# Kernel tuning notes

Measured on AMD Instinct MI355X. Metric: run time of the kernel, lower is better.

The kernel has to match this reference:

```python
import jax, jax.numpy as jnp
import numpy as np


def _conv(x, w, b):
    # stride-2, pad-1 3x3 conv, NCHW/OIHW
    y = jax.lax.conv_general_dilated(x, w, (2, 2), [(1, 1), (1, 1)],
                                     dimension_numbers=('NCHW', 'OIHW', 'NCHW'))
    return y + b[None, :, None, None]


def _bn(x, g, b, eps=1e-5):
    # BatchNorm2d in training mode: batch statistics over (N, H, W)
    m = x.mean((0, 2, 3), keepdims=True)
    v = x.var((0, 2, 3), keepdims=True)
    return (x - m) * jax.lax.rsqrt(v + eps) * g[None, :, None, None] + b[None, :, None, None]


def setup_inputs() -> dict:
    key = jax.random.key(0)
    ks = iter(jax.random.split(key, 64))
    def rn(shape, scale):
        return jax.random.normal(next(ks), shape, jnp.float32) * scale
    d = {}
    d['img'] = jax.random.normal(next(ks), (64, 3, 128, 128), jnp.float32)
    d['qst'] = jax.random.normal(next(ks), (64, 11), jnp.float32)
    cin = 3
    for i in range(1, 5):
        d[f'cw{i}'] = rn((24, cin, 3, 3), 1.0 / np.sqrt(cin * 9))
        d[f'cb{i}'] = jnp.zeros((24,), jnp.float32)
        d[f'bg{i}'] = jnp.ones((24,), jnp.float32)
        d[f'bb{i}'] = jnp.zeros((24,), jnp.float32)
        cin = 24
    gdims = [63, 256, 256, 256]
    for i in range(1, 5):
        d[f'gw{i}'] = rn((gdims[i - 1], 256), 1.0 / np.sqrt(gdims[i - 1]))
        d[f'gb{i}'] = jnp.zeros((256,), jnp.float32)
    fdims = [(256, 256), (256, 256), (256, 10)]
    for i, (a, b) in enumerate(fdims, 1):
        d[f'fw{i}'] = rn((a, b), 1.0 / np.sqrt(a))
        d[f'fb{i}'] = jnp.zeros((b,), jnp.float32)
    return d


def reference(img, qst,
              cw1, cb1, bg1, bb1, cw2, cb2, bg2, bb2,
              cw3, cb3, bg3, bb3, cw4, cb4, bg4, bb4,
              gw1, gb1, gw2, gb2, gw3, gb3, gw4, gb4,
              fw1, fb1, fw2, fb2, fw3, fb3):
    x = img
    for cw, cb, bg, bb in ((cw1, cb1, bg1, bb1), (cw2, cb2, bg2, bb2),
                           (cw3, cb3, bg3, bb3), (cw4, cb4, bg4, bb4)):
        x = _bn(jax.nn.relu(_conv(x, cw, cb)), bg, bb)
    B, C, H, W = x.shape
    n = H * W  # number of objects (feature-map cells)
    o = x.reshape(B, C, n).transpose(0, 2, 1)  # [B, n, 24]
    idx = jnp.arange(n)
    coords = jnp.stack([idx // H, idx % W], axis=1).astype(x.dtype)  # [n, 2]
    o = jnp.concatenate([o, jnp.broadcast_to(coords, (B, n, 2))], axis=2)  # [B, n, 26]
    # First G layer fused over the pairwise concat cat([x_i, x_j, qst], -1) @ gw1:
    # x_i[b,a,c] = o[b,c], x_j[b,a,c] = o[b,a] -> split gw1 into the three blocks.
    Wi, Wj, Wq = gw1[:26], gw1[26:52], gw1[52:]
    h = jax.nn.relu((o @ Wi)[:, None, :, :]
                    + (o @ Wj)[:, :, None, :]
                    + (qst @ Wq + gb1)[:, None, None, :])  # [B, n, n, 256]
    h = jax.nn.relu(h @ gw2 + gb2)
    h = jax.nn.relu(h @ gw3 + gb3)
    h = jax.nn.relu(h @ gw4 + gb4)
    g = h.sum((1, 2))  # sum over all n*n pairs -> [B, 256]
    f = jax.nn.relu(g @ fw1 + fb1)
    f = jax.nn.relu(f @ fw2 + fb2)  # Dropout(0.5) is identity at inference
    return jax.nn.softmax(f @ fw3 + fb3, axis=-1)
```

## Files before the change

kernel.cpp:

```cpp
#include <hip/hip_runtime.h>
#include <hip/hip_bf16.h>

typedef __attribute__((ext_vector_type(8))) short bf16x8_t;
typedef __attribute__((ext_vector_type(4))) float f32x4_t;

__device__ __forceinline__ unsigned bfr(float x) {
  unsigned u = __builtin_bit_cast(unsigned, x);
  return (u + 0x7fffu + ((u >> 16) & 1u)) >> 16;
}
__device__ __forceinline__ unsigned pk2(float lo, float hi) {
  return bfr(lo) | (bfr(hi) << 16);
}

template<int CIN, int H, int COG, bool BNIN>
__global__ __launch_bounds__(256) void convk(
    const float* __restrict__ x, const float* __restrict__ wgt,
    const float* __restrict__ bias,
    const float* __restrict__ instats,
    const float* __restrict__ ing, const float* __restrict__ inb,
    float* __restrict__ y, float* __restrict__ stats)
{
  constexpr int W = H, HO = H / 2, WO = W / 2;
  constexpr int PXB = (COG == 1) ? 256 : 64;
  constexpr int OHS = PXB / WO;
  constexpr int SPB = HO / OHS;
  constexpr int NR = 2 * OHS + 1;
  constexpr int TW = W + 1;
  constexpr int NSTG = NR * W;
  constexpr int NCO = 24 / COG;

  __shared__ float tile[2][NR][TW];
  __shared__ float scb[CIN], shb[CIN];
  __shared__ float sred[24], sqd[24];

  const int tid = threadIdx.x;
  const int b = blockIdx.x / SPB;
  const int strip = blockIdx.x % SPB;
  const int oh0 = strip * OHS;
  const int lane = tid & 63;

  if (BNIN && tid < CIN) {
    const float cnt = 64.f * H * W;
    const float m = instats[tid] / cnt;
    const float v = instats[24 + tid] / cnt - m * m;
    const float s = rsqrtf(v + 1e-5f) * ing[tid];
    scb[tid] = s;
    shb[tid] = inb[tid] - m * s;
  }
  if (tid < 24) { sred[tid] = 0.f; sqd[tid] = 0.f; }
  for (int i = tid; i < 2 * NR; i += 256)
    tile[i / NR][i % NR][0] = 0.f;
  __syncthreads();

  const int px = (COG == 1) ? tid : lane;
  const int ow = px % WO;
  const int ohl = px / WO;
  const int oh = oh0 + ohl;
  const int cb = (COG == 1) ? 0
               : __builtin_amdgcn_readfirstlane(tid >> 6) * NCO;

  float acc[NCO];
  #pragma unroll
  for (int n = 0; n < NCO; ++n) acc[n] = bias[cb + n];

  {
    const float sc = BNIN ? scb[0] : 1.f, sh = BNIN ? shb[0] : 0.f;
    #pragma unroll
    for (int idx = tid; idx < NSTG; idx += 256) {
      const int c = idx % W, rl = idx / W;
      const int ih = oh0 * 2 - 1 + rl;
      float v = 0.f;
      if (ih >= 0)
        v = x[((size_t)(b * CIN + 0) * H + ih) * W + c] * sc + sh;
      tile[0][rl][c + 1] = v;
    }
  }
  __syncthreads();

  for (int ci = 0; ci < CIN; ++ci) {
    if (ci + 1 < CIN) {
      const float sc = BNIN ? scb[ci + 1] : 1.f, sh = BNIN ? shb[ci + 1] : 0.f;
      #pragma unroll
      for (int idx = tid; idx < NSTG; idx += 256) {
        const int c = idx % W, rl = idx / W;
        const int ih = oh0 * 2 - 1 + rl;
        float v = 0.f;
        if (ih >= 0)
          v = x[((size_t)(b * CIN + ci + 1) * H + ih) * W + c] * sc + sh;
        tile[(ci + 1) & 1][rl][c + 1] = v;
      }
    }
    float tp[9];
    #pragma unroll
    for (int r = 0; r < 3; ++r)
      #pragma unroll
      for (int s = 0; s < 3; ++s)
        tp[r * 3 + s] = tile[ci & 1][2 * ohl + r][2 * ow + s];
    #pragma unroll
    for (int n = 0; n < NCO; ++n) {
      const float* wp = wgt + (size_t)((cb + n) * CIN + ci) * 9;
      float a = acc[n];
      #pragma unroll
      for (int k = 0; k < 9; ++k) a += tp[k] * wp[k];
      acc[n] = a;
    }
    __syncthreads();
  }

  #pragma unroll
  for (int n = 0; n < NCO; ++n) {
    const float v = fmaxf(acc[n], 0.f);
    acc[n] = v;
    y[((size_t)(b * 24 + cb + n) * HO + oh) * WO + ow] = v;
  }
  #pragma unroll
  for (int n = 0; n < NCO; ++n) {
    float v = acc[n], q = v * v;
    #pragma unroll
    for (int d = 1; d < 64; d <<= 1) {
      v += __shfl_xor(v, d, 64);
      q += __shfl_xor(q, d, 64);
    }
    if (lane == 0) {
      atomicAdd(&sred[cb + n], v);
      atomicAdd(&sqd[cb + n], q);
    }
  }
  __syncthreads();
  if (tid < 24) {
    atomicAdd(&stats[tid], sred[tid]);
    atomicAdd(&stats[24 + tid], sqd[tid]);
  }
}

__global__ __launch_bounds__(256) void build_ab(
    const float* __restrict__ x4, const float* __restrict__ stats4,
    const float* __restrict__ g4, const float* __restrict__ b4,
    const float* __restrict__ gw1, const float* __restrict__ gb1,
    const float* __restrict__ qst,
    float* __restrict__ A, float* __restrict__ Bm, float* __restrict__ Cq)
{
  const int bp = blockIdx.x;
  const int b = bp >> 6, p = bp & 63;
  const int t = threadIdx.x;
  __shared__ float o[26];
  if (t < 24) {
    const float m = stats4[t] * (1.f / 4096.f);
    const float v = stats4[24 + t] * (1.f / 4096.f) - m * m;
    const float sc = rsqrtf(v + 1e-5f) * g4[t];
    const float sh = b4[t] - m * sc;
    o[t] = x4[(size_t)(b * 24 + t) * 64 + p] * sc + sh;
  } else if (t == 24) o[24] = (float)(p >> 3);
  else if (t == 25) o[25] = (float)(p & 7);
  __syncthreads();
  float a = 0.f, bb2 = 0.f;
  #pragma unroll
  for (int c = 0; c < 26; ++c) {
    a   += o[c] * gw1[c * 256 + t];
    bb2 += o[c] * gw1[(26 + c) * 256 + t];
  }
  A[(size_t)bp * 256 + t]  = a;
  Bm[(size_t)bp * 256 + t] = bb2;
  if (p == 0) {
    float cqa = gb1[t];
    #pragma unroll
    for (int c = 0; c < 11; ++c)
      cqa += qst[b * 11 + c] * gw1[(52 + c) * 256 + t];
    Cq[b * 256 + t] = cqa;
  }
}

__global__ __launch_bounds__(256) void wt_convert3(
    const float* __restrict__ W2, const float* __restrict__ W3,
    const float* __restrict__ W4, unsigned short* __restrict__ wt)
{
  const int which = blockIdx.x >> 6;
  const float* W = which == 0 ? W2 : which == 1 ? W3 : W4;
  unsigned short* o = wt + (size_t)which * 65536;
  __shared__ float ts[32][33];
  const int blk = blockIdx.x & 63;
  const int k0 = (blk & 7) * 32, n0 = (blk >> 3) * 32;
  const int t = threadIdx.x;
  const int r = t >> 3, c4 = (t & 7) * 4;
  const float4 v = *(const float4*)(W + (size_t)(k0 + r) * 256 + n0 + c4);
  ts[r][c4 + 0] = v.x; ts[r][c4 + 1] = v.y;
  ts[r][c4 + 2] = v.z; ts[r][c4 + 3] = v.w;
  __syncthreads();
  uint2 ov;
  ov.x = pk2(ts[c4 + 0][r], ts[c4 + 1][r]);
  ov.y = pk2(ts[c4 + 2][r], ts[c4 + 3][r]);
  *(uint2*)(o + (size_t)(n0 + r) * 256 + k0 + c4) = ov;
}

__global__ __launch_bounds__(256) void pair_mfma(
    const float* __restrict__ A, const float* __restrict__ Bm,
    const float* __restrict__ Cq,
    const unsigned short* __restrict__ wtall,
    const float* __restrict__ b2, const float* __restrict__ b3,
    const float* __restrict__ b4,
    float* __restrict__ Gpart)
{
  __shared__ __align__(16) unsigned short hsm[64 * 256];
  __shared__ __align__(16) unsigned short wbuf[2][256 * 40];
  __shared__ float gpart[256];

  const int tid = threadIdx.x;
  int bid = blockIdx.x;
  bid = (bid & 7) * 512 + (bid >> 3);
  const int b = bid >> 6, local = bid & 63;
  const int lane = tid & 63, cg = tid >> 6;
  const int l15 = lane & 15, l4 = lane >> 4;
  char* hbase = (char*)hsm;

  const int r0 = tid >> 2, ss = tid & 3;

  {
    const int m = tid >> 2, seg = tid & 3;
    const float* Ar = A  + (size_t)(b * 64 + m) * 256 + seg * 64;
    const float* Br = Bm + (size_t)(b * 64 + local) * 256 + seg * 64;
    const float* Cr = Cq + (size_t)b * 256 + seg * 64;
    #pragma unroll
    for (int it = 0; it < 8; ++it) {
      const float4 a0 = *(const float4*)(Ar + it * 8);
      const float4 a1 = *(const float4*)(Ar + it * 8 + 4);
      const float4 b0 = *(const float4*)(Br + it * 8);
      const float4 b1 = *(const float4*)(Br + it * 8 + 4);
      const float4 c0 = *(const float4*)(Cr + it * 8);
      const float4 c1 = *(const float4*)(Cr + it * 8 + 4);
      uint4 pk;
      pk.x = pk2(fmaxf(a0.x + b0.x + c0.x, 0.f), fmaxf(a0.y + b0.y + c0.y, 0.f));
      pk.y = pk2(fmaxf(a0.z + b0.z + c0.z, 0.f), fmaxf(a0.w + b0.w + c0.w, 0.f));
      pk.z = pk2(fmaxf(a1.x + b1.x + c1.x, 0.f), fmaxf(a1.y + b1.y + c1.y, 0.f));
      pk.w = pk2(fmaxf(a1.z + b1.z + c1.z, 0.f), fmaxf(a1.w + b1.w + c1.w, 0.f));
      const int kb = seg * 128 + it * 16;
      *(uint4*)(hbase + (size_t)m * 512 + (kb ^ ((m & 7) << 4))) = pk;
    }
  }

  {
    #pragma unroll
    for (int q = 0; q < 4; ++q) {
      const int n = r0 + q * 64;
      const uint4 v = *(const uint4*)(wtall + (size_t)n * 256 + ss * 8);
      *(uint4*)(wbuf[0] + n * 40 + ss * 8) = v;
    }
  }
  __syncthreads();

  const float* bs3[3] = {b2, b3, b4};

  for (int layer = 0; layer < 3; ++layer) {
    f32x4_t acc[4][4];
    #pragma unroll
    for (int a = 0; a < 4; ++a) {
      const float4 bv = *(const float4*)(bs3[layer] + cg * 64 + a * 16 + l4 * 4);
      #pragma unroll
      for (int t = 0; t < 4; ++t) {
        acc[a][t][0] = bv.x; acc[a][t][1] = bv.y;
        acc[a][t][2] = bv.z; acc[a][t][3] = bv.w;
      }
    }
    for (int ks = 0; ks < 8; ++ks) {
      const int c = layer * 8 + ks;
      uint4 p0, p1, p2, p3;
      if (c + 1 < 24) {
        const unsigned short* src =
            wtall + (size_t)((c + 1) >> 3) * 65536 + ((c + 1) & 7) * 32;
        p0 = *(const uint4*)(src + (size_t)(r0)       * 256 + ss * 8);
        p1 = *(const uint4*)(src + (size_t)(r0 + 64)  * 256 + ss * 8);
        p2 = *(const uint4*)(src + (size_t)(r0 + 128) * 256 + ss * 8);
        p3 = *(const uint4*)(src + (size_t)(r0 + 192) * 256 + ss * 8);
      }
      bf16x8_t bf[4];
      #pragma unroll
      for (int t = 0; t < 4; ++t) {
        const int row = t * 16 + l15;
        const int kb = ks * 64 + l4 * 16;
        bf[t] = *(const bf16x8_t*)(hbase + (size_t)row * 512 + (kb ^ ((row & 7) << 4)));
      }
      const unsigned short* wrd = wbuf[c & 1];
      #pragma unroll
      for (int a = 0; a < 4; ++a) {
        const bf16x8_t af = *(const bf16x8_t*)(wrd + (cg * 64 + a * 16 + l15) * 40 + l4 * 8);
        #pragma unroll
        for (int t = 0; t < 4; ++t)
          acc[a][t] = __builtin_amdgcn_mfma_f32_16x16x32_bf16(af, bf[t], acc[a][t], 0, 0, 0);
      }
      if (c + 1 < 24) {
        unsigned short* wb = wbuf[(c + 1) & 1];
        *(uint4*)(wb + (r0)       * 40 + ss * 8) = p0;
        *(uint4*)(wb + (r0 + 64)  * 40 + ss * 8) = p1;
        *(uint4*)(wb + (r0 + 128) * 40 + ss * 8) = p2;
        *(uint4*)(wb + (r0 + 192) * 40 + ss * 8) = p3;
      }
      __syncthreads();
    }

    if (layer < 2) {
      #pragma unroll
      for (int a = 0; a < 4; ++a) {
        #pragma unroll
        for (int t = 0; t < 4; ++t) {
          const int row = t * 16 + l15;
          const int n0 = cg * 64 + a * 16 + l4 * 4;
          uint2 v;
          v.x = pk2(fmaxf(acc[a][t][0], 0.f), fmaxf(acc[a][t][1], 0.f));
          v.y = pk2(fmaxf(acc[a][t][2], 0.f), fmaxf(acc[a][t][3], 0.f));
          *(uint2*)(hbase + (size_t)row * 512 + ((n0 * 2) ^ ((row & 7) << 4))) = v;
        }
      }
      __syncthreads();
    } else {
      #pragma unroll
      for (int a = 0; a < 4; ++a) {
        f32x4_t s;
        s[0] = s[1] = s[2] = s[3] = 0.f;
        #pragma unroll
        for (int t = 0; t < 4; ++t) {
          s[0] += fmaxf(acc[a][t][0], 0.f);
          s[1] += fmaxf(acc[a][t][1], 0.f);
          s[2] += fmaxf(acc[a][t][2], 0.f);
          s[3] += fmaxf(acc[a][t][3], 0.f);
        }
        #pragma unroll
        for (int d = 1; d < 16; d <<= 1) {
          s[0] += __shfl_xor(s[0], d, 64);
          s[1] += __shfl_xor(s[1], d, 64);
          s[2] += __shfl_xor(s[2], d, 64);
          s[3] += __shfl_xor(s[3], d, 64);
        }
        if (l15 == 0)
          *(f32x4_t*)(&gpart[cg * 64 + a * 16 + l4 * 4]) = s;
      }
      __syncthreads();
      Gpart[(size_t)(b * 64 + local) * 256 + tid] = gpart[tid];
    }
  }
}

__global__ __launch_bounds__(256) void reduce_g(
    const float* __restrict__ Gpart, float* __restrict__ g)
{
  const int b = blockIdx.x, t = threadIdx.x;
  float s = 0.f;
  for (int j = 0; j < 64; ++j) s += Gpart[(size_t)(b * 64 + j) * 256 + t];
  g[b * 256 + t] = s;
}

__global__ __launch_bounds__(256) void fnet(
    const float* __restrict__ g,
    const float* __restrict__ fw1, const float* __restrict__ fb1,
    const float* __restrict__ fw2, const float* __restrict__ fb2,
    const float* __restrict__ fw3, const float* __restrict__ fb3,
    float* __restrict__ out)
{
  const int b = blockIdx.x, t = threadIdx.x;
  __shared__ float s0[256], s1[256], lg[10];
  s0[t] = g[b * 256 + t];
  __syncthreads();
  float acc = fb1[t];
  for (int k = 0; k < 256; ++k) acc += s0[k] * fw1[k * 256 + t];
  s1[t] = fmaxf(acc, 0.f);
  __syncthreads();
  acc = fb2[t];
  for (int k = 0; k < 256; ++k) acc += s1[k] * fw2[k * 256 + t];
  s0[t] = fmaxf(acc, 0.f);
  __syncthreads();
  if (t < 10) {
    float a = fb3[t];
    for (int k = 0; k < 256; ++k) a += s0[k] * fw3[k * 10 + t];
    lg[t] = a;
  }
  __syncthreads();
  if (t == 0) {
    float m = lg[0];
    for (int c = 1; c < 10; ++c) m = fmaxf(m, lg[c]);
    float e[10], sum = 0.f;
    for (int c = 0; c < 10; ++c) { e[c] = expf(lg[c] - m); sum += e[c]; }
    const float inv = 1.f / sum;
    for (int c = 0; c < 10; ++c) out[b * 10 + c] = e[c] * inv;
  }
}

extern "C" void kernel_launch(void* const* d_in, const int* in_sizes, int n_in,
                              void* d_out, int out_size, void* d_ws, size_t ws_size,
                              hipStream_t stream)
{
  const float* img = (const float*)d_in[0];
  const float* qst = (const float*)d_in[1];
  const float* cw[4] = {(const float*)d_in[2],  (const float*)d_in[6],
                        (const float*)d_in[10], (const float*)d_in[14]};
  const float* cb[4] = {(const float*)d_in[3],  (const float*)d_in[7],
                        (const float*)d_in[11], (const float*)d_in[15]};
  const float* bg[4] = {(const float*)d_in[4],  (const float*)d_in[8],
                        (const float*)d_in[12], (const float*)d_in[16]};
  const float* bb[4] = {(const float*)d_in[5],  (const float*)d_in[9],
                        (const float*)d_in[13], (const float*)d_in[17]};
  const float* gw1 = (const float*)d_in[18];
  const float* gb1 = (const float*)d_in[19];
  const float* gw2 = (const float*)d_in[20];
  const float* gb2 = (const float*)d_in[21];
  const float* gw3 = (const float*)d_in[22];
  const float* gb3 = (const float*)d_in[23];
  const float* gw4 = (const float*)d_in[24];
  const float* gb4 = (const float*)d_in[25];
  const float* fw1 = (const float*)d_in[26];
  const float* fb1 = (const float*)d_in[27];
  const float* fw2 = (const float*)d_in[28];
  const float* fb2 = (const float*)d_in[29];
  const float* fw3 = (const float*)d_in[30];
  const float* fb3 = (const float*)d_in[31];
  float* out = (float*)d_out;

  float* ws    = (float*)d_ws;
  float* x1    = ws;
  float* x2    = x1 + 6291456;
  float* x3    = x2 + 1572864;
  float* x4    = x3 + 393216;
  float* Abuf  = x4 + 98304;
  float* Bbuf  = Abuf + 1048576;
  float* Cqb   = Bbuf + 1048576;
  float* Gpart = Cqb + 16384;
  float* gbuf  = Gpart + 1048576;
  float* stats = gbuf + 16384;
  unsigned short* wtb = (unsigned short*)(stats + 192);

  hipMemsetAsync(stats, 0, 192 * sizeof(float), stream);

  convk<3, 128, 1, false><<<1024, 256, 0, stream>>>(
      img, cw[0], cb[0], nullptr, nullptr, nullptr, x1, stats + 0);
  convk<24, 64, 4, true><<<1024, 256, 0, stream>>>(
      x1, cw[1], cb[1], stats + 0, bg[0], bb[0], x2, stats + 48);
  convk<24, 32, 4, true><<<256, 256, 0, stream>>>(
      x2, cw[2], cb[2], stats + 48, bg[1], bb[1], x3, stats + 96);
  convk<24, 16, 4, true><<<64, 256, 0, stream>>>(
      x3, cw[3], cb[3], stats + 96, bg[2], bb[2], x4, stats + 144);

  build_ab<<<4096, 256, 0, stream>>>(x4, stats + 144, bg[3], bb[3], gw1,
                                     gb1, qst, Abuf, Bbuf, Cqb);
  wt_convert3<<<192, 256, 0, stream>>>(gw2, gw3, gw4, wtb);

  pair_mfma<<<4096, 256, 0, stream>>>(Abuf, Bbuf, Cqb, wtb, gb2, gb3, gb4,
                                      Gpart);
  reduce_g<<<64, 256, 0, stream>>>(Gpart, gbuf);
  fnet<<<64, 256, 0, stream>>>(gbuf, fw1, fb1, fw2, fb2, fw3, fb3, out);
}
```

Baseline: 572.4 us.

## Pre-swizzle MFMA weight fragments, batch build_ab rows, fuse reduce_g into fnet

Weights for layers 2-4 are now converted into a per-k-slice MFMA fragment layout, so pair_mfma streams each slice with contiguous uint4 copies and reads A-fragments directly by lane, with no padded strided rows. build_ab handles 8 objects per block, so each gw1 weight load is reused across eight rows and the launch shrinks from 4096 blocks to 512. The separate reduce_g kernel is folded into fnet, which drops one launch and one intermediate buffer. The weight conversion now runs first in the stream, and the new LDS fragment layout may have different bank-conflict behaviour.

```diff
diff --git a/kernel.cpp b/kernel.cpp
--- a/kernel.cpp
+++ b/kernel.cpp
@@ -141,27 +141,40 @@
     float* __restrict__ A, float* __restrict__ Bm, float* __restrict__ Cq)
 {
   const int bp = blockIdx.x;
-  const int b = bp >> 6, p = bp & 63;
+  const int b = bp >> 3, pg = bp & 7;
   const int t = threadIdx.x;
-  __shared__ float o[26];
-  if (t < 24) {
-    const float m = stats4[t] * (1.f / 4096.f);
-    const float v = stats4[24 + t] * (1.f / 4096.f) - m * m;
-    const float sc = rsqrtf(v + 1e-5f) * g4[t];
-    const float sh = b4[t] - m * sc;
-    o[t] = x4[(size_t)(b * 24 + t) * 64 + p] * sc + sh;
-  } else if (t == 24) o[24] = (float)(p >> 3);
-  else if (t == 25) o[25] = (float)(p & 7);
-  __syncthreads();
-  float a = 0.f, bb2 = 0.f;
+  __shared__ float o[8][26];
+  if (t < 208) {
+    const int r = t / 26, c = t % 26;
+    if (c < 24) {
+      const float m = stats4[c] * (1.f / 4096.f);
+      const float v = stats4[24 + c] * (1.f / 4096.f) - m * m;
+      const float sc = rsqrtf(v + 1e-5f) * g4[c];
+      const float sh = b4[c] - m * sc;
+      o[r][c] = x4[(size_t)(b * 24 + c) * 64 + pg * 8 + r] * sc + sh;
+    } else if (c == 24) o[r][24] = (float)pg;
+    else                o[r][25] = (float)r;
+  }
+  __syncthreads();
+  float accA[8], accB[8];
+  #pragma unroll
+  for (int r = 0; r < 8; ++r) { accA[r] = 0.f; accB[r] = 0.f; }
   #pragma unroll
   for (int c = 0; c < 26; ++c) {
-    a   += o[c] * gw1[c * 256 + t];
-    bb2 += o[c] * gw1[(26 + c) * 256 + t];
-  }
-  A[(size_t)bp * 256 + t]  = a;
-  Bm[(size_t)bp * 256 + t] = bb2;
-  if (p == 0) {
+    const float wi = gw1[c * 256 + t];
+    const float wj = gw1[(26 + c) * 256 + t];
+    #pragma unroll
+    for (int r = 0; r < 8; ++r) {
+      accA[r] += o[r][c] * wi;
+      accB[r] += o[r][c] * wj;
+    }
+  }
+  #pragma unroll
+  for (int r = 0; r < 8; ++r) {
+    A[(size_t)(b * 64 + pg * 8 + r) * 256 + t]  = accA[r];
+    Bm[(size_t)(b * 64 + pg * 8 + r) * 256 + t] = accB[r];
+  }
+  if (pg == 0) {
     float cqa = gb1[t];
     #pragma unroll
     for (int c = 0; c < 11; ++c)
@@ -170,26 +183,28 @@
   }
 }
 
-__global__ __launch_bounds__(256) void wt_convert3(
+__global__ __launch_bounds__(256) void wt_convert_frag(
     const float* __restrict__ W2, const float* __restrict__ W3,
     const float* __restrict__ W4, unsigned short* __restrict__ wt)
 {
-  const int which = blockIdx.x >> 6;
-  const float* W = which == 0 ? W2 : which == 1 ? W3 : W4;
-  unsigned short* o = wt + (size_t)which * 65536;
-  __shared__ float ts[32][33];
-  const int blk = blockIdx.x & 63;
-  const int k0 = (blk & 7) * 32, n0 = (blk >> 3) * 32;
+  const int c = blockIdx.x;
+  const int layer = c >> 3, ks = c & 7;
+  const float* W = layer == 0 ? W2 : layer == 1 ? W3 : W4;
   const int t = threadIdx.x;
-  const int r = t >> 3, c4 = (t & 7) * 4;
-  const float4 v = *(const float4*)(W + (size_t)(k0 + r) * 256 + n0 + c4);
-  ts[r][c4 + 0] = v.x; ts[r][c4 + 1] = v.y;
-  ts[r][c4 + 2] = v.z; ts[r][c4 + 3] = v.w;
-  __syncthreads();
-  uint2 ov;
-  ov.x = pk2(ts[c4 + 0][r], ts[c4 + 1][r]);
-  ov.y = pk2(ts[c4 + 2][r], ts[c4 + 3][r]);
-  *(uint2*)(o + (size_t)(n0 + r) * 256 + k0 + c4) = ov;
+  #pragma unroll
+  for (int q = 0; q < 4; ++q) {
+    const int f = q * 256 + t;
+    const int cg = f >> 8, a = (f >> 6) & 3, ln = f & 63;
+    const int n = cg * 64 + a * 16 + (ln & 15);
+    const int k0 = ks * 32 + (ln >> 4) * 8;
+    float w[8];
+    #pragma unroll
+    for (int u = 0; u < 8; ++u) w[u] = W[(size_t)(k0 + u) * 256 + n];
+    uint4 ov;
+    ov.x = pk2(w[0], w[1]); ov.y = pk2(w[2], w[3]);
+    ov.z = pk2(w[4], w[5]); ov.w = pk2(w[6], w[7]);
+    *(uint4*)(wt + (size_t)c * 8192 + (size_t)f * 8) = ov;
+  }
 }
 
 __global__ __launch_bounds__(256) void pair_mfma(
@@ -201,7 +216,7 @@
     float* __restrict__ Gpart)
 {
   __shared__ __align__(16) unsigned short hsm[64 * 256];
-  __shared__ __align__(16) unsigned short wbuf[2][256 * 40];
+  __shared__ __align__(16) unsigned short wbuf[2][8192];
   __shared__ float gpart[256];
 
   const int tid = threadIdx.x;
@@ -211,8 +226,6 @@
   const int lane = tid & 63, cg = tid >> 6;
   const int l15 = lane & 15, l4 = lane >> 4;
   char* hbase = (char*)hsm;
-
-  const int r0 = tid >> 2, ss = tid & 3;
 
   {
     const int m = tid >> 2, seg = tid & 3;
@@ -238,12 +251,11 @@
   }
 
   {
-    #pragma unroll
-    for (int q = 0; q < 4; ++q) {
-      const int n = r0 + q * 64;
-      const uint4 v = *(const uint4*)(wtall + (size_t)n * 256 + ss * 8);
-      *(uint4*)(wbuf[0] + n * 40 + ss * 8) = v;
-    }
+    const uint4* src = (const uint4*)wtall;
+    uint4* dst = (uint4*)wbuf[0];
+    #pragma unroll
+    for (int q = 0; q < 4; ++q)
+      dst[q * 256 + tid] = src[q * 256 + tid];
   }
   __syncthreads();
 
@@ -264,12 +276,11 @@
       const int c = layer * 8 + ks;
       uint4 p0, p1, p2, p3;
       if (c + 1 < 24) {
-        const unsigned short* src =
-            wtall + (size_t)((c + 1) >> 3) * 65536 + ((c + 1) & 7) * 32;
-        p0 = *(const uint4*)(src + (size_t)(r0)       * 256 + ss * 8);
-        p1 = *(const uint4*)(src + (size_t)(r0 + 64)  * 256 + ss * 8);
-        p2 = *(const uint4*)(src + (size_t)(r0 + 128) * 256 + ss * 8);
-        p3 = *(const uint4*)(src + (size_t)(r0 + 192) * 256 + ss * 8);
+        const uint4* src = (const uint4*)wtall + (size_t)(c + 1) * 1024;
+        p0 = src[0 * 256 + tid];
+        p1 = src[1 * 256 + tid];
+        p2 = src[2 * 256 + tid];
+        p3 = src[3 * 256 + tid];
       }
       bf16x8_t bf[4];
       #pragma unroll
@@ -281,17 +292,17 @@
       const unsigned short* wrd = wbuf[c & 1];
       #pragma unroll
       for (int a = 0; a < 4; ++a) {
-        const bf16x8_t af = *(const bf16x8_t*)(wrd + (cg * 64 + a * 16 + l15) * 40 + l4 * 8);
+        const bf16x8_t af = *(const bf16x8_t*)(wrd + ((size_t)(cg * 4 + a) * 64 + lane) * 8);
         #pragma unroll
         for (int t = 0; t < 4; ++t)
           acc[a][t] = __builtin_amdgcn_mfma_f32_16x16x32_bf16(af, bf[t], acc[a][t], 0, 0, 0);
       }
       if (c + 1 < 24) {
-        unsigned short* wb = wbuf[(c + 1) & 1];
-        *(uint4*)(wb + (r0)       * 40 + ss * 8) = p0;
-        *(uint4*)(wb + (r0 + 64)  * 40 + ss * 8) = p1;
-        *(uint4*)(wb + (r0 + 128) * 40 + ss * 8) = p2;
-        *(uint4*)(wb + (r0 + 192) * 40 + ss * 8) = p3;
+        uint4* wb = (uint4*)wbuf[(c + 1) & 1];
+        wb[0 * 256 + tid] = p0;
+        wb[1 * 256 + tid] = p1;
+        wb[2 * 256 + tid] = p2;
+        wb[3 * 256 + tid] = p3;
       }
       __syncthreads();
     }
@@ -338,17 +349,8 @@
   }
 }
 
-__global__ __launch_bounds__(256) void reduce_g(
-    const float* __restrict__ Gpart, float* __restrict__ g)
-{
-  const int b = blockIdx.x, t = threadIdx.x;
-  float s = 0.f;
-  for (int j = 0; j < 64; ++j) s += Gpart[(size_t)(b * 64 + j) * 256 + t];
-  g[b * 256 + t] = s;
-}
-
 __global__ __launch_bounds__(256) void fnet(
-    const float* __restrict__ g,
+    const float* __restrict__ Gpart,
     const float* __restrict__ fw1, const float* __restrict__ fb1,
     const float* __restrict__ fw2, const float* __restrict__ fb2,
     const float* __restrict__ fw3, const float* __restrict__ fb3,
@@ -356,7 +358,10 @@
 {
   const int b = blockIdx.x, t = threadIdx.x;
   __shared__ float s0[256], s1[256], lg[10];
-  s0[t] = g[b * 256 + t];
+  float g = 0.f;
+  for (int j = 0; j < 64; ++j)
+    g += Gpart[(size_t)(b * 64 + j) * 256 + t];
+  s0[t] = g;
   __syncthreads();
   float acc = fb1[t];
   for (int k = 0; k < 256; ++k) acc += s0[k] * fw1[k * 256 + t];
@@ -421,11 +426,12 @@
   float* Bbuf  = Abuf + 1048576;
   float* Cqb   = Bbuf + 1048576;
   float* Gpart = Cqb + 16384;
-  float* gbuf  = Gpart + 1048576;
-  float* stats = gbuf + 16384;
+  float* stats = Gpart + 1048576;
   unsigned short* wtb = (unsigned short*)(stats + 192);
 
   hipMemsetAsync(stats, 0, 192 * sizeof(float), stream);
+
+  wt_convert_frag<<<24, 256, 0, stream>>>(gw2, gw3, gw4, wtb);
 
   convk<3, 128, 1, false><<<1024, 256, 0, stream>>>(
       img, cw[0], cb[0], nullptr, nullptr, nullptr, x1, stats + 0);
@@ -436,12 +442,10 @@
   convk<24, 16, 4, true><<<64, 256, 0, stream>>>(
       x3, cw[3], cb[3], stats + 96, bg[2], bb[2], x4, stats + 144);
 
-  build_ab<<<4096, 256, 0, stream>>>(x4, stats + 144, bg[3], bb[3], gw1,
-                                     gb1, qst, Abuf, Bbuf, Cqb);
-  wt_convert3<<<192, 256, 0, stream>>>(gw2, gw3, gw4, wtb);
+  build_ab<<<512, 256, 0, stream>>>(x4, stats + 144, bg[3], bb[3], gw1,
+                                    gb1, qst, Abuf, Bbuf, Cqb);
 
   pair_mfma<<<4096, 256, 0, stream>>>(Abuf, Bbuf, Cqb, wtb, gb2, gb3, gb4,
                                       Gpart);
-  reduce_g<<<64, 256, 0, stream>>>(Gpart, gbuf);
-  fnet<<<64, 256, 0, stream>>>(gbuf, fw1, fb1, fw2, fb2, fw3, fb3, out);
-}
+  fnet<<<64, 256, 0, stream>>>(Gpart, fw1, fb1, fw2, fb2, fw3, fb3, out);
+}
```

Measured after the change: 556.0 us. -2.9%, faster.
